# Kernel tuning notes

Measured on AMD Instinct MI355X. Metric: run time of the kernel, lower is better.

The kernel has to match this reference:

```python
import jax, jax.numpy as jnp
import numpy as np

NUM_ITEMS = 100000
FEAT = 64
EMB = 64
B = 16384
H = 50


def setup_inputs() -> dict:
    key = jax.random.key(0)
    ks = jax.random.split(key, 16)
    inp = {
        'hist_indices': jax.random.randint(ks[0], (B, H), 0, NUM_ITEMS),
        'hist_features': jax.random.normal(ks[1], (B, H, FEAT), dtype=jnp.float32),
        'hist_ratings': jax.random.uniform(ks[2], (B, H), dtype=jnp.float32) * 4.0 + 1.0,
        'target_indices': jax.random.randint(ks[3], (B,), 0, NUM_ITEMS),
        'target_features': jax.random.normal(ks[4], (B, FEAT), dtype=jnp.float32),
        # parameters
        'embed_table': jax.random.normal(ks[5], (NUM_ITEMS, EMB), dtype=jnp.float32) * 0.05,
        'fusion_w': jax.random.normal(ks[6], (EMB + FEAT, EMB), dtype=jnp.float32) * 0.05,
        'fusion_b': jnp.zeros((EMB,), dtype=jnp.float32),
        'w1': jax.random.normal(ks[7], (EMB * 2, 64), dtype=jnp.float32) * 0.05,
        'b1': jnp.zeros((64,), dtype=jnp.float32),
        'w2': jax.random.normal(ks[8], (64, 32), dtype=jnp.float32) * 0.05,
        'b2': jnp.zeros((32,), dtype=jnp.float32),
        'w3': jax.random.normal(ks[9], (32, 1), dtype=jnp.float32) * 0.05,
        'b3': jnp.zeros((1,), dtype=jnp.float32),
    }
    return inp


def _item_rep(idx, feats, embed_table, fusion_w, fusion_b):
    emb = embed_table[idx]  # gather: (..., EMB)
    x = jnp.concatenate([emb, feats], axis=-1)
    return jax.nn.relu(x @ fusion_w + fusion_b)


def reference(hist_indices, hist_features, hist_ratings, target_indices, target_features,
              embed_table, fusion_w, fusion_b, w1, b1, w2, b2, w3, b3):
    # user vector: weighted-sum pooling over history
    hist_reps = _item_rep(hist_indices, hist_features, embed_table, fusion_w, fusion_b)  # (B,H,EMB)
    weights = (hist_ratings - 3.0)[..., None]  # (B,H,1)
    user_vec = jnp.sum(hist_reps * weights, axis=1) / (jnp.sum(jnp.abs(weights), axis=1) + 1e-8)  # (B,EMB)
    # target representation
    target_rep = _item_rep(target_indices, target_features, embed_table, fusion_w, fusion_b)  # (B,EMB)
    # rating MLP (dropout is identity at inference)
    x = jnp.concatenate([user_vec, target_rep], axis=-1)  # (B, 2*EMB)
    h = jax.nn.relu(x @ w1 + b1)
    h = jax.nn.relu(h @ w2 + b2)
    pred = h @ w3 + b3  # (B,1)
    return pred.squeeze(-1)
```

## Files before the change

kernel.cpp:

```cpp
#include <hip/hip_runtime.h>

#define NB 16384
#define NH 50

typedef __attribute__((ext_vector_type(4))) float        f32x4;
typedef __attribute__((ext_vector_type(8))) short        s16x8;
typedef __attribute__((ext_vector_type(4))) unsigned int u32x4;


__device__ __forceinline__ unsigned rne16(float x) {
  unsigned u = __float_as_uint(x);
  return (u + 0x7FFFu + ((u >> 16) & 1u)) >> 16;
}
__device__ __forceinline__ unsigned pack_hi(float x0, float x1, float& r0, float& r1) {
  const unsigned h0 = rne16(x0), h1 = rne16(x1);
  r0 = x0 - __uint_as_float(h0 << 16);
  r1 = x1 - __uint_as_float(h1 << 16);
  return h0 | (h1 << 16);
}
__device__ __forceinline__ unsigned pack_rne(float x0, float x1) {
  return rne16(x0) | (rne16(x1) << 16);
}
__device__ __forceinline__ void cvt8(const f32x4 a, const f32x4 b, u32x4& hi, u32x4& lo) {
  float r0, r1;
  hi[0] = pack_hi(a[0], a[1], r0, r1); lo[0] = pack_rne(r0, r1);
  hi[1] = pack_hi(a[2], a[3], r0, r1); lo[1] = pack_rne(r0, r1);
  hi[2] = pack_hi(b[0], b[1], r0, r1); lo[2] = pack_rne(r0, r1);
  hi[3] = pack_hi(b[2], b[3], r0, r1); lo[3] = pack_rne(r0, r1);
}

__global__ __launch_bounds__(256) void wprep_k(const float* __restrict__ fw,
                                               unsigned* __restrict__ bfrag) {
  const int d = blockIdx.x * 256 + threadIdx.x;
  const int j = d & 3, l = (d >> 2) & 63, f = d >> 8;
  const int sp = f & 1, nt = (f >> 1) & 3, ks = f >> 3;
  const int n  = nt * 16 + (l & 15);
  const int k0 = ks * 32 + (l >> 4) * 8 + 2 * j;
  const float w0 = fw[k0 * 64 + n], w1 = fw[(k0 + 1) * 64 + n];
  const unsigned h0 = rne16(w0), h1 = rne16(w1);
  unsigned dw;
  if (sp == 0) dw = h0 | (h1 << 16);
  else {
    const float r0 = w0 - __uint_as_float(h0 << 16);
    const float r1 = w1 - __uint_as_float(h1 << 16);
    dw = rne16(r0) | (rne16(r1) << 16);
  }
  bfrag[d] = dw;
}

__global__ __launch_bounds__(256, 2) void pool_mfma_k(
    const int* __restrict__ hidx, const float* __restrict__ hfeat,
    const float* __restrict__ hrat, const int* __restrict__ tidx,
    const float* __restrict__ tfeat, const float* __restrict__ table,
    const float* __restrict__ fb, const unsigned* __restrict__ bfrag,
    float* __restrict__ user_vec, float* __restrict__ target_rep)
{
  const int l  = threadIdx.x & 63;
  const int wv = threadIdx.x >> 6;
  const int wave = (blockIdx.x << 2) + wv;
  const int lm = l & 15, lg = l >> 4;
  const int b0 = wave, b1 = wave + 8192;

  const int r_l = (l < NH) ? l : (NH - 1);
  int idxv0 = hidx[(size_t)b0 * NH + r_l];
  int idxv1 = hidx[(size_t)b1 * NH + r_l];
  float rat0 = (l < NH) ? (hrat[(size_t)b0 * NH + l] - 3.0f) : 0.f;
  float rat1 = (l < NH) ? (hrat[(size_t)b1 * NH + l] - 3.0f) : 0.f;
  if (l == NH) { idxv0 = tidx[b0]; idxv1 = tidx[b1]; }

  u32x4 B[4][4][2];
#pragma unroll
  for (int ks = 0; ks < 4; ++ks)
#pragma unroll
    for (int nt = 0; nt < 4; ++nt)
#pragma unroll
      for (int sp = 0; sp < 2; ++sp) {
        const int f = (ks << 3) | (nt << 1) | sp;
        B[ks][nt][sp] = *(const u32x4*)(bfrag + ((size_t)f * 64 + l) * 4);
      }
  float bias[4];
#pragma unroll
  for (int nt = 0; nt < 4; ++nt) bias[nt] = fb[nt * 16 + lm];

#pragma unroll
  for (int rep = 0; rep < 2; ++rep) {
    const int   b      = rep ? b1 : b0;
    const int   myidx  = rep ? idxv1 : idxv0;
    const float rw_all = rep ? rat1 : rat0;

    float den = fabsf(rw_all);
#pragma unroll
    for (int s = 32; s >= 1; s >>= 1) den += __shfl_xor(den, s, 64);

    float uacc[4] = {0.f, 0.f, 0.f, 0.f};
    float trep[4] = {0.f, 0.f, 0.f, 0.f};

#pragma unroll
    for (int m = 0; m < 4; ++m) {
      const int r = m * 16 + lm;
      const int idxm = __shfl(myidx, (r < NH) ? r : ((r == NH) ? NH : (NH - 1)), 64);
      const float* fp = (r < NH) ? (hfeat + ((size_t)b * NH + r) * 64)
                      : (r == NH) ? (tfeat + (size_t)b * 64)
                                  : (hfeat + ((size_t)b * NH + (NH - 1)) * 64);
      const float* ep = table + (size_t)idxm * 64;
      f32x4 q0 = *(const f32x4*)(ep + lg * 8);
      f32x4 q1 = *(const f32x4*)(ep + lg * 8 + 4);
      f32x4 q2 = *(const f32x4*)(ep + 32 + lg * 8);
      f32x4 q3 = *(const f32x4*)(ep + 32 + lg * 8 + 4);
      f32x4 q4 = *(const f32x4*)(fp + lg * 8);
      f32x4 q5 = *(const f32x4*)(fp + lg * 8 + 4);
      f32x4 q6 = *(const f32x4*)(fp + 32 + lg * 8);
      f32x4 q7 = *(const f32x4*)(fp + 32 + lg * 8 + 4);
      u32x4 ahi[4], alo[4];
      cvt8(q0, q1, ahi[0], alo[0]);
      cvt8(q2, q3, ahi[1], alo[1]);
      cvt8(q4, q5, ahi[2], alo[2]);
      cvt8(q6, q7, ahi[3], alo[3]);

      f32x4 acc[4];
#pragma unroll
      for (int nt = 0; nt < 4; ++nt) {
        const float bv = bias[nt];
        acc[nt] = (f32x4){bv, bv, bv, bv};
      }
#pragma unroll
      for (int ks = 0; ks < 4; ++ks) {
        const s16x8 ah = __builtin_bit_cast(s16x8, ahi[ks]);
        const s16x8 al = __builtin_bit_cast(s16x8, alo[ks]);
#pragma unroll
        for (int nt = 0; nt < 4; ++nt) {
          const s16x8 bh = __builtin_bit_cast(s16x8, B[ks][nt][0]);
          const s16x8 bl = __builtin_bit_cast(s16x8, B[ks][nt][1]);
          acc[nt] = __builtin_amdgcn_mfma_f32_16x16x32_bf16(ah, bh, acc[nt], 0, 0, 0);
          acc[nt] = __builtin_amdgcn_mfma_f32_16x16x32_bf16(al, bh, acc[nt], 0, 0, 0);
          acc[nt] = __builtin_amdgcn_mfma_f32_16x16x32_bf16(ah, bl, acc[nt], 0, 0, 0);
        }
      }
#pragma unroll
      for (int nt = 0; nt < 4; ++nt) {
#pragma unroll
        for (int e = 0; e < 4; ++e) {
          const float repv = fmaxf(acc[nt][e], 0.f);
          const int   rr   = m * 16 + lg * 4 + e;
          const float w    = __shfl(rw_all, rr, 64);
          uacc[nt] = fmaf(w, repv, uacc[nt]);
          if (m == 3 && e == 2) trep[nt] = repv;
        }
      }
    }

#pragma unroll
    for (int nt = 0; nt < 4; ++nt) {
      uacc[nt] += __shfl_xor(uacc[nt], 16, 64);
      uacc[nt] += __shfl_xor(uacc[nt], 32, 64);
    }
    const float dinv = den + 1e-8f;
    const float usel = (lg == 0) ? uacc[0] : (lg == 1) ? uacc[1]
                     : (lg == 2) ? uacc[2] : uacc[3];
    user_vec[(size_t)b * 64 + l] = usel / dinv;
    if (l < 16) {
      float* tp = target_rep + (size_t)b * 64 + l;
      tp[0]  = trep[0];
      tp[16] = trep[1];
      tp[32] = trep[2];
      tp[48] = trep[3];
    }
  }
}

__global__ __launch_bounds__(256) void mlp_k(
    const float* __restrict__ user_vec, const float* __restrict__ target_rep,
    const float* __restrict__ w1, const float* __restrict__ b1,
    const float* __restrict__ w2, const float* __restrict__ b2,
    const float* __restrict__ w3, const float* __restrict__ b3,
    float* __restrict__ out)
{
  __shared__ alignas(16) float s_w1[128 * 64];
  __shared__ alignas(16) float s_w2[64 * 32];
  __shared__ float s_w3[32];
  __shared__ alignas(16) float s_x[4][128];
  __shared__ alignas(16) float s_h1[4][64];
  const int tid = threadIdx.x;
  for (int i = tid; i < 128 * 64; i += 256) s_w1[i] = w1[i];
  for (int i = tid; i < 64 * 32;  i += 256) s_w2[i] = w2[i];
  if (tid < 32) s_w3[tid] = w3[tid];
  __syncthreads();

  const int t  = tid & 63;
  const int wv = tid >> 6;
  const int nwaves = gridDim.x << 2;
  const float b1t = b1[t];
  const float bb3 = b3[0];
  const int n2 = t & 31;
  const float b2n = b2[n2];
  for (int b = (blockIdx.x << 2) + wv; b < NB; b += nwaves) {
    s_x[wv][t]      = user_vec[(size_t)b * 64 + t];
    s_x[wv][64 + t] = target_rep[(size_t)b * 64 + t];
    float a0 = b1t, a1 = 0.f, a2 = 0.f, a3 = 0.f;
#pragma unroll
    for (int k4 = 0; k4 < 32; ++k4) {
      float4 x = *reinterpret_cast<const float4*>(&s_x[wv][k4 * 4]);
      a0 = fmaf(x.x, s_w1[(4 * k4 + 0) * 64 + t], a0);
      a1 = fmaf(x.y, s_w1[(4 * k4 + 1) * 64 + t], a1);
      a2 = fmaf(x.z, s_w1[(4 * k4 + 2) * 64 + t], a2);
      a3 = fmaf(x.w, s_w1[(4 * k4 + 3) * 64 + t], a3);
    }
    s_h1[wv][t] = fmaxf((a0 + a1) + (a2 + a3), 0.f);
    float c0 = b2n, c1 = 0.f, c2 = 0.f, c3 = 0.f;
#pragma unroll
    for (int k4 = 0; k4 < 16; ++k4) {
      float4 x = *reinterpret_cast<const float4*>(&s_h1[wv][k4 * 4]);
      c0 = fmaf(x.x, s_w2[(4 * k4 + 0) * 32 + n2], c0);
      c1 = fmaf(x.y, s_w2[(4 * k4 + 1) * 32 + n2], c1);
      c2 = fmaf(x.z, s_w2[(4 * k4 + 2) * 32 + n2], c2);
      c3 = fmaf(x.w, s_w2[(4 * k4 + 3) * 32 + n2], c3);
    }
    const float h2 = fmaxf((c0 + c1) + (c2 + c3), 0.f);
    float p = (t < 32) ? h2 * s_w3[n2] : 0.f;
#pragma unroll
    for (int m = 32; m >= 1; m >>= 1) p += __shfl_xor(p, m, 64);
    if (t == 0) out[b] = p + bb3;
  }
}

extern "C" void kernel_launch(void* const* d_in, const int* in_sizes, int n_in,
                              void* d_out, int out_size, void* d_ws, size_t ws_size,
                              hipStream_t stream) {
  const int*   hidx  = (const int*)  d_in[0];
  const float* hfeat = (const float*)d_in[1];
  const float* hrat  = (const float*)d_in[2];
  const int*   tidx  = (const int*)  d_in[3];
  const float* tfeat = (const float*)d_in[4];
  const float* table = (const float*)d_in[5];
  const float* fw    = (const float*)d_in[6];
  const float* fb    = (const float*)d_in[7];
  const float* w1    = (const float*)d_in[8];
  const float* b1    = (const float*)d_in[9];
  const float* w2    = (const float*)d_in[10];
  const float* b2    = (const float*)d_in[11];
  const float* w3    = (const float*)d_in[12];
  const float* b3    = (const float*)d_in[13];
  float* out = (float*)d_out;
  float* ws  = (float*)d_ws;
  unsigned* bfrag   = (unsigned*)ws;
  float* user_vec   = ws + 6400000;
  float* target_rep = ws + 7448576;

  hipLaunchKernelGGL(wprep_k, dim3(32), dim3(256), 0, stream, fw, bfrag);
  hipLaunchKernelGGL(pool_mfma_k, dim3(2048), dim3(256), 0, stream,
                     hidx, hfeat, hrat, tidx, tfeat, table, fb, bfrag,
                     user_vec, target_rep);
  hipLaunchKernelGGL(mlp_k, dim3(512), dim3(256), 0, stream,
                     user_vec, target_rep, w1, b1, w2, b2, w3, b3, out);
}
```

Baseline: 118.5 us.

## Software-pipeline gather loads across tiles and cheapen bf16 split conversion

Flattens the two per-wave batch rows and four row tiles into one eight-step loop. It double-buffers the gathered embedding and feature loads so the next tile's global loads are issued before the current tile's MFMA work. It also replaces the rounding-based hi/lo bf16 split with a truncated hi part plus a hardware-packed RNE conversion of the residual, which cuts integer ALU work. The cost is higher register pressure from holding two sets of 8 float4 tiles, and a small change in how the hi/lo split rounds.

```diff
diff --git a/kernel.cpp b/kernel.cpp
--- a/kernel.cpp
+++ b/kernel.cpp
@@ -1,4 +1,5 @@
 #include <hip/hip_runtime.h>
+#include <hip/hip_bf16.h>
 
 #define NB 16384
 #define NH 50
@@ -12,21 +13,31 @@
   unsigned u = __float_as_uint(x);
   return (u + 0x7FFFu + ((u >> 16) & 1u)) >> 16;
 }
-__device__ __forceinline__ unsigned pack_hi(float x0, float x1, float& r0, float& r1) {
-  const unsigned h0 = rne16(x0), h1 = rne16(x1);
-  r0 = x0 - __uint_as_float(h0 << 16);
-  r1 = x1 - __uint_as_float(h1 << 16);
-  return h0 | (h1 << 16);
-}
-__device__ __forceinline__ unsigned pack_rne(float x0, float x1) {
-  return rne16(x0) | (rne16(x1) << 16);
-}
-__device__ __forceinline__ void cvt8(const f32x4 a, const f32x4 b, u32x4& hi, u32x4& lo) {
-  float r0, r1;
-  hi[0] = pack_hi(a[0], a[1], r0, r1); lo[0] = pack_rne(r0, r1);
-  hi[1] = pack_hi(a[2], a[3], r0, r1); lo[1] = pack_rne(r0, r1);
-  hi[2] = pack_hi(b[0], b[1], r0, r1); lo[2] = pack_rne(r0, r1);
-  hi[3] = pack_hi(b[2], b[3], r0, r1); lo[3] = pack_rne(r0, r1);
+
+__device__ __forceinline__ unsigned pk_bf16(float r0, float r1) {
+  __hip_bfloat162 h = __float22bfloat162_rn(make_float2(r0, r1));
+  unsigned u;
+  __builtin_memcpy(&u, &h, 4);
+  return u;
+}
+
+__device__ __forceinline__ void cvt8t(const f32x4 a, const f32x4 b, u32x4& hi, u32x4& lo) {
+  unsigned ha[8]; float r[8];
+#pragma unroll
+  for (int i = 0; i < 4; ++i) {
+    const unsigned ua = __float_as_uint(a[i]) & 0xFFFF0000u;
+    ha[i] = ua; r[i] = a[i] - __uint_as_float(ua);
+  }
+#pragma unroll
+  for (int i = 0; i < 4; ++i) {
+    const unsigned ub = __float_as_uint(b[i]) & 0xFFFF0000u;
+    ha[4 + i] = ub; r[4 + i] = b[i] - __uint_as_float(ub);
+  }
+#pragma unroll
+  for (int p = 0; p < 4; ++p) {
+    hi[p] = ha[2 * p + 1] | (ha[2 * p] >> 16);
+    lo[p] = pk_bf16(r[2 * p], r[2 * p + 1]);
+  }
 }
 
 __global__ __launch_bounds__(256) void wprep_k(const float* __restrict__ fw,
@@ -82,88 +93,103 @@
 #pragma unroll
   for (int nt = 0; nt < 4; ++nt) bias[nt] = fb[nt * 16 + lm];
 
-#pragma unroll
-  for (int rep = 0; rep < 2; ++rep) {
-    const int   b      = rep ? b1 : b0;
-    const int   myidx  = rep ? idxv1 : idxv0;
+  auto load_tile = [&](int i, f32x4* q) {
+    const int rep = i >> 2, m = i & 3;
+    const int bb  = rep ? b1 : b0;
+    const int mi  = rep ? idxv1 : idxv0;
+    const int r   = m * 16 + lm;
+    const int sel = (r <= NH) ? r : (NH - 1);
+    const int idxm = __shfl(mi, sel, 64);
+    const float* fp = (r < NH) ? (hfeat + ((size_t)bb * NH + r) * 64)
+                    : (r == NH) ? (tfeat + (size_t)bb * 64)
+                                : (hfeat + ((size_t)bb * NH + (NH - 1)) * 64);
+    const float* ep = table + (size_t)idxm * 64;
+    q[0] = *(const f32x4*)(ep + lg * 8);
+    q[1] = *(const f32x4*)(ep + lg * 8 + 4);
+    q[2] = *(const f32x4*)(ep + 32 + lg * 8);
+    q[3] = *(const f32x4*)(ep + 32 + lg * 8 + 4);
+    q[4] = *(const f32x4*)(fp + lg * 8);
+    q[5] = *(const f32x4*)(fp + lg * 8 + 4);
+    q[6] = *(const f32x4*)(fp + 32 + lg * 8);
+    q[7] = *(const f32x4*)(fp + 32 + lg * 8 + 4);
+  };
+
+  f32x4 qA[8], qB[8];
+  load_tile(0, qA);
+
+  float uacc[4] = {0.f, 0.f, 0.f, 0.f};
+  float trep[4] = {0.f, 0.f, 0.f, 0.f};
+
+#pragma unroll
+  for (int i = 0; i < 8; ++i) {
+    const int rep = i >> 2, m = i & 3;
+    f32x4* qc = (i & 1) ? qB : qA;
+    f32x4* qn = (i & 1) ? qA : qB;
+
+    u32x4 ahi[4], alo[4];
+    cvt8t(qc[0], qc[1], ahi[0], alo[0]);
+    cvt8t(qc[2], qc[3], ahi[1], alo[1]);
+    cvt8t(qc[4], qc[5], ahi[2], alo[2]);
+    cvt8t(qc[6], qc[7], ahi[3], alo[3]);
+
+    if (i < 7) load_tile(i + 1, qn);
+
+    f32x4 acc[4];
+#pragma unroll
+    for (int nt = 0; nt < 4; ++nt) {
+      const float bv = bias[nt];
+      acc[nt] = (f32x4){bv, bv, bv, bv};
+    }
+#pragma unroll
+    for (int ks = 0; ks < 4; ++ks) {
+      const s16x8 ah = __builtin_bit_cast(s16x8, ahi[ks]);
+      const s16x8 al = __builtin_bit_cast(s16x8, alo[ks]);
+#pragma unroll
+      for (int nt = 0; nt < 4; ++nt) {
+        const s16x8 bh = __builtin_bit_cast(s16x8, B[ks][nt][0]);
+        const s16x8 bl = __builtin_bit_cast(s16x8, B[ks][nt][1]);
+        acc[nt] = __builtin_amdgcn_mfma_f32_16x16x32_bf16(ah, bh, acc[nt], 0, 0, 0);
+        acc[nt] = __builtin_amdgcn_mfma_f32_16x16x32_bf16(al, bh, acc[nt], 0, 0, 0);
+        acc[nt] = __builtin_amdgcn_mfma_f32_16x16x32_bf16(ah, bl, acc[nt], 0, 0, 0);
+      }
+    }
+
     const float rw_all = rep ? rat1 : rat0;
-
-    float den = fabsf(rw_all);
-#pragma unroll
-    for (int s = 32; s >= 1; s >>= 1) den += __shfl_xor(den, s, 64);
-
-    float uacc[4] = {0.f, 0.f, 0.f, 0.f};
-    float trep[4] = {0.f, 0.f, 0.f, 0.f};
-
-#pragma unroll
-    for (int m = 0; m < 4; ++m) {
-      const int r = m * 16 + lm;
-      const int idxm = __shfl(myidx, (r < NH) ? r : ((r == NH) ? NH : (NH - 1)), 64);
-      const float* fp = (r < NH) ? (hfeat + ((size_t)b * NH + r) * 64)
-                      : (r == NH) ? (tfeat + (size_t)b * 64)
-                                  : (hfeat + ((size_t)b * NH + (NH - 1)) * 64);
-      const float* ep = table + (size_t)idxm * 64;
-      f32x4 q0 = *(const f32x4*)(ep + lg * 8);
-      f32x4 q1 = *(const f32x4*)(ep + lg * 8 + 4);
-      f32x4 q2 = *(const f32x4*)(ep + 32 + lg * 8);
-      f32x4 q3 = *(const f32x4*)(ep + 32 + lg * 8 + 4);
-      f32x4 q4 = *(const f32x4*)(fp + lg * 8);
-      f32x4 q5 = *(const f32x4*)(fp + lg * 8 + 4);
-      f32x4 q6 = *(const f32x4*)(fp + 32 + lg * 8);
-      f32x4 q7 = *(const f32x4*)(fp + 32 + lg * 8 + 4);
-      u32x4 ahi[4], alo[4];
-      cvt8(q0, q1, ahi[0], alo[0]);
-      cvt8(q2, q3, ahi[1], alo[1]);
-      cvt8(q4, q5, ahi[2], alo[2]);
-      cvt8(q6, q7, ahi[3], alo[3]);
-
-      f32x4 acc[4];
+#pragma unroll
+    for (int e = 0; e < 4; ++e) {
+      const int rr = m * 16 + lg * 4 + e;
+      const float w = __shfl(rw_all, rr, 64);
 #pragma unroll
       for (int nt = 0; nt < 4; ++nt) {
-        const float bv = bias[nt];
-        acc[nt] = (f32x4){bv, bv, bv, bv};
-      }
-#pragma unroll
-      for (int ks = 0; ks < 4; ++ks) {
-        const s16x8 ah = __builtin_bit_cast(s16x8, ahi[ks]);
-        const s16x8 al = __builtin_bit_cast(s16x8, alo[ks]);
-#pragma unroll
-        for (int nt = 0; nt < 4; ++nt) {
-          const s16x8 bh = __builtin_bit_cast(s16x8, B[ks][nt][0]);
-          const s16x8 bl = __builtin_bit_cast(s16x8, B[ks][nt][1]);
-          acc[nt] = __builtin_amdgcn_mfma_f32_16x16x32_bf16(ah, bh, acc[nt], 0, 0, 0);
-          acc[nt] = __builtin_amdgcn_mfma_f32_16x16x32_bf16(al, bh, acc[nt], 0, 0, 0);
-          acc[nt] = __builtin_amdgcn_mfma_f32_16x16x32_bf16(ah, bl, acc[nt], 0, 0, 0);
-        }
-      }
+        const float repv = fmaxf(acc[nt][e], 0.f);
+        uacc[nt] = fmaf(w, repv, uacc[nt]);
+        if (m == 3 && e == 2) trep[nt] = repv;
+      }
+    }
+
+    if (m == 3) {
+      float den = fabsf(rw_all);
+#pragma unroll
+      for (int s = 32; s >= 1; s >>= 1) den += __shfl_xor(den, s, 64);
 #pragma unroll
       for (int nt = 0; nt < 4; ++nt) {
-#pragma unroll
-        for (int e = 0; e < 4; ++e) {
-          const float repv = fmaxf(acc[nt][e], 0.f);
-          const int   rr   = m * 16 + lg * 4 + e;
-          const float w    = __shfl(rw_all, rr, 64);
-          uacc[nt] = fmaf(w, repv, uacc[nt]);
-          if (m == 3 && e == 2) trep[nt] = repv;
-        }
-      }
-    }
-
-#pragma unroll
-    for (int nt = 0; nt < 4; ++nt) {
-      uacc[nt] += __shfl_xor(uacc[nt], 16, 64);
-      uacc[nt] += __shfl_xor(uacc[nt], 32, 64);
-    }
-    const float dinv = den + 1e-8f;
-    const float usel = (lg == 0) ? uacc[0] : (lg == 1) ? uacc[1]
-                     : (lg == 2) ? uacc[2] : uacc[3];
-    user_vec[(size_t)b * 64 + l] = usel / dinv;
-    if (l < 16) {
-      float* tp = target_rep + (size_t)b * 64 + l;
-      tp[0]  = trep[0];
-      tp[16] = trep[1];
-      tp[32] = trep[2];
-      tp[48] = trep[3];
+        uacc[nt] += __shfl_xor(uacc[nt], 16, 64);
+        uacc[nt] += __shfl_xor(uacc[nt], 32, 64);
+      }
+      const int bb = rep ? b1 : b0;
+      const float dinv = den + 1e-8f;
+      const float usel = (lg == 0) ? uacc[0] : (lg == 1) ? uacc[1]
+                       : (lg == 2) ? uacc[2] : uacc[3];
+      user_vec[(size_t)bb * 64 + l] = usel / dinv;
+      if (l < 16) {
+        float* tp = target_rep + (size_t)bb * 64 + l;
+        tp[0]  = trep[0];
+        tp[16] = trep[1];
+        tp[32] = trep[2];
+        tp[48] = trep[3];
+      }
+#pragma unroll
+      for (int nt = 0; nt < 4; ++nt) { uacc[nt] = 0.f; trep[nt] = 0.f; }
     }
   }
 }
```

New measurement: 126.4 us. +6.7%, slower.
